# Kernel tuning notes

Hardware: AMD Instinct MI355X
Metric: run time of the kernel (lower is better)

## Reference

```python
import jax, jax.numpy as jnp
import numpy as np

HIDDEN = 4544
N_HEADS = 71
HEAD_DIM = 64
SEQ = 2048
ROPE_BASE = 10000.0


def _rope_cos_sin(seq_len, dim, base=ROPE_BASE):
    inv_freq = 1.0 / (base ** (jnp.arange(0, dim, 2, dtype=jnp.float32) / dim))
    t = jnp.arange(seq_len, dtype=jnp.float32)
    freqs = jnp.einsum('i,j->ij', t, inv_freq)          # [s, dim/2]
    emb = jnp.concatenate([freqs, freqs], axis=-1)      # [s, dim]
    return jnp.cos(emb), jnp.sin(emb)


def _rotate_half(x):
    x1, x2 = jnp.split(x, 2, axis=-1)
    return jnp.concatenate([-x2, x1], axis=-1)


def _apply_rope(x, cos, sin):
    # x: [..., s, d]; cos/sin: [s, d] broadcast over leading dims
    return x * cos + _rotate_half(x) * sin


def setup_inputs() -> dict:
    key = jax.random.key(0)
    k1, k2, k3 = jax.random.split(key, 3)
    hidden_states = jax.random.normal(k1, (1, 1, SEQ, HIDDEN), dtype=jnp.float32) * 0.02
    qkv_weight = jax.random.normal(k2, ((N_HEADS + 2) * HEAD_DIM, HIDDEN), dtype=jnp.float32) * 0.02
    dense_weight = jax.random.normal(k3, (HIDDEN, HIDDEN), dtype=jnp.float32) * 0.02
    # causal additive mask, same construction as the torch module (triu of -1e5)
    mask = jnp.triu(jnp.full((SEQ, SEQ), -100000.0, dtype=jnp.float32), k=1)[None, None]
    return {
        'hidden_states': hidden_states,
        'qkv_weight': qkv_weight,
        'dense_weight': dense_weight,
        'attention_mask': mask,
    }


def reference(hidden_states, qkv_weight, dense_weight, attention_mask):
    b = hidden_states.shape[0]
    s = hidden_states.shape[2]
    x = hidden_states[:, 0]                                   # [b, s, H]

    # fused QKV projection (no bias): [b, s, (nH+2)*d]
    fused = jnp.einsum('bsh,oh->bso', x, qkv_weight)

    q = fused[..., : N_HEADS * HEAD_DIM]
    q = q.reshape(b, s, N_HEADS, HEAD_DIM).transpose(0, 2, 1, 3)   # [b, nH, s, d]
    k = fused[..., N_HEADS * HEAD_DIM : (N_HEADS + 1) * HEAD_DIM]  # [b, s, d] (single KV head, MQA)
    v = fused[..., (N_HEADS + 1) * HEAD_DIM :]                     # [b, s, d]

    cos, sin = _rope_cos_sin(s, HEAD_DIM)
    q = _apply_rope(q, cos, sin)
    k = _apply_rope(k, cos, sin)

    scale = 1.0 / np.sqrt(HEAD_DIM).astype(np.float32)
    scores = jnp.einsum('bhqd,bkd->bhqk', q, k) * scale            # [b, nH, s, s]
    scores = scores + attention_mask
    attn = jax.nn.softmax(scores, axis=-1)
    out = jnp.einsum('bhqk,bkd->bhqd', attn, v)                    # [b, nH, s, d]

    out = out.transpose(0, 2, 1, 3).reshape(b, s, N_HEADS * HEAD_DIM)  # concat heads
    out = jnp.einsum('bsh,oh->bso', out, dense_weight)             # dense projection
    return out[:, None]                                            # [b, 1, s, H]
```

## Files before the change

kernel.cpp:

```cpp
#include <hip/hip_runtime.h>

#define SEQ     2048
#define HIDDEN  4544
#define NHEAD   71
#define HD      64
#define QKV_OUT 4672

typedef __bf16    bf16;
typedef _Float16  f16;
typedef __bf16    bf16x8 __attribute__((ext_vector_type(8)));
typedef __bf16    bf16x4 __attribute__((ext_vector_type(4)));
typedef _Float16  f16x4  __attribute__((ext_vector_type(4)));
typedef float     f32x4  __attribute__((ext_vector_type(4)));

__device__ inline void gl2lds16(const void* g, void* ldsbase) {
  __builtin_amdgcn_global_load_lds(
      (const __attribute__((address_space(1))) unsigned int*)g,
      (__attribute__((address_space(3))) unsigned int*)ldsbase,
      16, 0, 0);
}

__global__ void cvt_f32_bf16_k(const float* __restrict__ in, bf16* __restrict__ out, int n4) {
  int i = blockIdx.x * blockDim.x + threadIdx.x;
  if (i >= n4) return;
  float4 f = ((const float4*)in)[i];
  bf16x4 o;
  o[0] = (bf16)f.x; o[1] = (bf16)f.y; o[2] = (bf16)f.z; o[3] = (bf16)f.w;
  *(bf16x4*)(out + (size_t)i * 4) = o;
}

__global__ __launch_bounds__(256) void gemm_bt_k(const bf16* __restrict__ A,
                                                 const bf16* __restrict__ B,
                                                 float* __restrict__ C,
                                                 int K, int Nmat, int ldc) {
  __shared__ bf16 lA[2][128 * 32];
  __shared__ bf16 lB[2][128 * 32];
  const int t = threadIdx.x;
  const int lane = t & 63, w = t >> 6;
  const int m0 = blockIdx.x * 128, n0 = blockIdx.y * 128;
  const int wm = (w >> 1) * 64, wn = (w & 1) * 64;
  const int qi = lane & 15, grp = lane >> 4;

  const int r0 = t >> 2;
  const int c0 = (t & 3) * 8;
  const bf16* gA0 = A + (size_t)(m0 + r0) * K + c0;
  const bf16* gA1 = A + (size_t)(m0 + 64 + r0) * K + c0;
  int bR0 = n0 + r0;      if (bR0 >= Nmat) bR0 = Nmat - 1;
  int bR1 = n0 + 64 + r0; if (bR1 >= Nmat) bR1 = Nmat - 1;
  const bf16* gB0 = B + (size_t)bR0 * K + c0;
  const bf16* gB1 = B + (size_t)bR1 * K + c0;
  bf16* lA00 = &lA[0][0] + w * 512;
  bf16* lA01 = &lA[0][2048] + w * 512;
  bf16* lA10 = &lA[1][0] + w * 512;
  bf16* lA11 = &lA[1][2048] + w * 512;
  bf16* lB00 = &lB[0][0] + w * 512;
  bf16* lB01 = &lB[0][2048] + w * 512;
  bf16* lB10 = &lB[1][0] + w * 512;
  bf16* lB11 = &lB[1][2048] + w * 512;

  f32x4 acc[4][4] = {};
  for (int k0 = 0; k0 < K; k0 += 64) {
    __syncthreads();
    gl2lds16(gA0 + k0,      lA00);
    gl2lds16(gA1 + k0,      lA01);
    gl2lds16(gA0 + k0 + 32, lA10);
    gl2lds16(gA1 + k0 + 32, lA11);
    gl2lds16(gB0 + k0,      lB00);
    gl2lds16(gB1 + k0,      lB01);
    gl2lds16(gB0 + k0 + 32, lB10);
    gl2lds16(gB1 + k0 + 32, lB11);
    __syncthreads();
#pragma unroll
    for (int half = 0; half < 2; ++half) {
      bf16x8 af[4], bfv[4];
#pragma unroll
      for (int i = 0; i < 4; ++i)
        af[i] = *(const bf16x8*)&lA[half][(wm + i * 16 + qi) * 32 + grp * 8];
#pragma unroll
      for (int i = 0; i < 4; ++i)
        bfv[i] = *(const bf16x8*)&lB[half][(wn + i * 16 + qi) * 32 + grp * 8];
#pragma unroll
      for (int i = 0; i < 4; ++i)
#pragma unroll
        for (int j = 0; j < 4; ++j)
          acc[i][j] = __builtin_amdgcn_mfma_f32_16x16x32_bf16(af[i], bfv[j], acc[i][j], 0, 0, 0);
    }
  }

#pragma unroll
  for (int i = 0; i < 4; ++i) {
    const int row = m0 + wm + i * 16 + grp * 4;
#pragma unroll
    for (int j = 0; j < 4; ++j) {
      const int col = n0 + wn + j * 16 + qi;
      if (col < Nmat) {
#pragma unroll
        for (int r = 0; r < 4; ++r)
          C[(size_t)(row + r) * ldc + col] = acc[i][j][r];
      }
    }
  }
}

__global__ __launch_bounds__(256) void rope_q_k(const float* __restrict__ fused,
                                                bf16* __restrict__ Qb,
                                                float* __restrict__ cs_tab,
                                                float* __restrict__ sn_tab) {
  const int s = blockIdx.x, t = threadIdx.x;
  __shared__ float cs[64], sn[64];
  if (t < 64) {
    int i = t & 31;
    double invf = pow(10000.0, -(double)i / 32.0);
    double ang = (double)s * invf;
    float c = (float)cos(ang), n = (float)sin(ang);
    cs[t] = c; sn[t] = n;
    cs_tab[s * 64 + t] = c;
    sn_tab[s * 64 + t] = n;
  }
  __syncthreads();
  const float* row = fused + (size_t)s * QKV_OUT;
  for (int e = t; e < HIDDEN; e += 256) {
    int d = e & 63;
    float x = row[e], xp = row[e ^ 32];
    float rot = (d < 32) ? -xp : xp;
    Qb[(size_t)s * HIDDEN + e] = (bf16)((x * cs[d] + rot * sn[d]) * 0.125f);
  }
}

__global__ __launch_bounds__(64) void kvprep_k(const float* __restrict__ fused,
                                               const float* __restrict__ cs_tab,
                                               const float* __restrict__ sn_tab,
                                               bf16* __restrict__ Kf,
                                               f16* __restrict__ Vf) {
  const int t16 = blockIdx.x, lane = threadIdx.x;
  const int qi = lane & 15, grp = lane >> 4;
  const int s = t16 * 16 + qi;
  const float* krow = fused + (size_t)s * QKV_OUT + NHEAD * 64;
  const float* cs = cs_tab + s * 64;
  const float* sn = sn_tab + s * 64;
#pragma unroll
  for (int half = 0; half < 2; ++half) {
    bf16x8 o;
    const int d0 = half * 32 + grp * 8;
#pragma unroll
    for (int j = 0; j < 8; ++j) {
      int d = d0 + j;
      float x = krow[d], xp = krow[d ^ 32];
      float rot = (d < 32) ? -xp : xp;
      o[j] = (bf16)(x * cs[d] + rot * sn[d]);
    }
    *(bf16x8*)&Kf[(t16 * 2 + half) * 512 + lane * 8] = o;
  }
#pragma unroll
  for (int tt = 0; tt < 4; ++tt) {
    f16x4 o;
#pragma unroll
    for (int j = 0; j < 4; ++j)
      o[j] = (f16)fused[(size_t)(t16 * 16 + grp * 4 + j) * QKV_OUT + (NHEAD + 1) * 64 + tt * 16 + qi];
    *(f16x4*)&Vf[t16 * 1024 + tt * 256 + lane * 4] = o;
  }
}

__global__ __launch_bounds__(64) void attn_k(const bf16* __restrict__ Qb,
                                             const bf16* __restrict__ Kf,
                                             const f16*  __restrict__ Vf,
                                             bf16* __restrict__ Ao) {
  __shared__ float fl[2 * 16 * 68];
  const int h = blockIdx.y;
  const int b32 = gridDim.x - 1 - blockIdx.x;
  const int lane = threadIdx.x;
  const int qi = lane & 15, grp = lane >> 4;
  const int q0 = b32 * 32;
  const int lastT = b32 >> 1;

  bf16x8 qf[2][2];
#pragma unroll
  for (int qq = 0; qq < 2; ++qq) {
    const bf16* qb = Qb + (size_t)(q0 + qq * 16 + qi) * HIDDEN + h * 64 + grp * 8;
    qf[qq][0] = *(const bf16x8*)qb;
    qf[qq][1] = *(const bf16x8*)(qb + 32);
  }

  f32x4 o[2][4] = {};
  float l[2] = {0.f, 0.f};

  for (int kb = 0; kb <= lastT; ++kb) {
    const bf16* kfp = Kf + (size_t)kb * 4096 + lane * 8;
    bf16x8 kf[4][2];
#pragma unroll
    for (int kk = 0; kk < 4; ++kk) {
      kf[kk][0] = *(const bf16x8*)(kfp + kk * 1024);
      kf[kk][1] = *(const bf16x8*)(kfp + kk * 1024 + 512);
    }
    f32x4 s4[2][4];
#pragma unroll
    for (int qq = 0; qq < 2; ++qq)
#pragma unroll
      for (int kk = 0; kk < 4; ++kk) {
        f32x4 z = {};
        s4[qq][kk] = __builtin_amdgcn_mfma_f32_16x16x32_bf16(kf[kk][0], qf[qq][0], z, 0, 0, 0);
        s4[qq][kk] = __builtin_amdgcn_mfma_f32_16x16x32_bf16(kf[kk][1], qf[qq][1], s4[qq][kk], 0, 0, 0);
      }
    const f16* vfp = Vf + (size_t)kb * 4096 + lane * 4;
    f16x4 vf[4][4];
#pragma unroll
    for (int kk = 0; kk < 4; ++kk)
#pragma unroll
      for (int tt = 0; tt < 4; ++tt)
        vf[kk][tt] = *(const f16x4*)(vfp + kk * 1024 + tt * 256);

    if (kb == lastT) {
      const int dq = q0 - kb * 64 + qi;
#pragma unroll
      for (int qq = 0; qq < 2; ++qq)
#pragma unroll
        for (int kk = 0; kk < 4; ++kk)
#pragma unroll
          for (int r = 0; r < 4; ++r)
            if (kk * 16 + grp * 4 + r > dq + qq * 16) s4[qq][kk][r] = -1e30f;
    }
    f16x4 pf[2][4];
#pragma unroll
    for (int qq = 0; qq < 2; ++qq) {
      float ls = 0.f;
#pragma unroll
      for (int kk = 0; kk < 4; ++kk) {
        float p0 = __expf(s4[qq][kk][0]), p1 = __expf(s4[qq][kk][1]);
        float p2 = __expf(s4[qq][kk][2]), p3 = __expf(s4[qq][kk][3]);
        ls += (p0 + p1) + (p2 + p3);
        pf[qq][kk][0] = (f16)p0; pf[qq][kk][1] = (f16)p1;
        pf[qq][kk][2] = (f16)p2; pf[qq][kk][3] = (f16)p3;
      }
      l[qq] += ls;
    }
#pragma unroll
    for (int qq = 0; qq < 2; ++qq)
#pragma unroll
      for (int tt = 0; tt < 4; ++tt)
#pragma unroll
        for (int kk = 0; kk < 4; ++kk)
          o[qq][tt] = __builtin_amdgcn_mfma_f32_16x16x16f16(pf[qq][kk], vf[kk][tt], o[qq][tt], 0, 0, 0);
  }

#pragma unroll
  for (int qq = 0; qq < 2; ++qq) {
    float lq = l[qq];
    lq += __shfl_xor(lq, 16);
    lq += __shfl_xor(lq, 32);
    const float inv = 1.0f / lq;
    const float i0 = __shfl(inv, grp * 4 + 0);
    const float i1 = __shfl(inv, grp * 4 + 1);
    const float i2 = __shfl(inv, grp * 4 + 2);
    const float i3 = __shfl(inv, grp * 4 + 3);
    float* flq = fl + qq * 1088;
#pragma unroll
    for (int tt = 0; tt < 4; ++tt) {
      flq[(grp * 4 + 0) * 68 + tt * 16 + qi] = o[qq][tt][0] * i0;
      flq[(grp * 4 + 1) * 68 + tt * 16 + qi] = o[qq][tt][1] * i1;
      flq[(grp * 4 + 2) * 68 + tt * 16 + qi] = o[qq][tt][2] * i2;
      flq[(grp * 4 + 3) * 68 + tt * 16 + qi] = o[qq][tt][3] * i3;
    }
  }
  __syncthreads();
  const int row = lane >> 2, c0 = (lane & 3) * 16;
#pragma unroll
  for (int qq = 0; qq < 2; ++qq) {
    const float* flq = fl + qq * 1088;
    bf16x8 w0, w1;
#pragma unroll
    for (int j = 0; j < 8; ++j) {
      w0[j] = (bf16)flq[row * 68 + c0 + j];
      w1[j] = (bf16)flq[row * 68 + c0 + 8 + j];
    }
    bf16* ob = Ao + (size_t)(q0 + qq * 16 + row) * HIDDEN + h * 64 + c0;
    *(bf16x8*)ob = w0;
    *(bf16x8*)(ob + 8) = w1;
  }
}

extern "C" void kernel_launch(void* const* d_in, const int* in_sizes, int n_in,
                              void* d_out, int out_size, void* d_ws, size_t ws_size,
                              hipStream_t stream) {
  (void)in_sizes; (void)n_in; (void)out_size; (void)ws_size;
  const float* hs   = (const float*)d_in[0];
  const float* wqkv = (const float*)d_in[1];
  const float* wd   = (const float*)d_in[2];
  float* out = (float*)d_out;

  char* ws = (char*)d_ws;
  size_t off = 0;
  auto alloc = [&](size_t b) -> char* {
    char* p = ws + off;
    off += (b + 255) & ~(size_t)255;
    return p;
  };
  bf16* Xb     = (bf16*)alloc((size_t)SEQ * HIDDEN * 2);
  bf16* Wqb    = (bf16*)alloc((size_t)QKV_OUT * HIDDEN * 2);
  bf16* Wdb    = (bf16*)alloc((size_t)HIDDEN * HIDDEN * 2);
  float* fused = (float*)alloc((size_t)SEQ * QKV_OUT * 4);
  bf16* Qb     = (bf16*)alloc((size_t)SEQ * HIDDEN * 2);
  bf16* Kf     = (bf16*)alloc((size_t)(SEQ / 16) * 1024 * 2);
  f16*  Vf     = (f16*)alloc((size_t)(SEQ / 16) * 1024 * 2);
  float* cs_tab = (float*)alloc((size_t)SEQ * 64 * 4);
  float* sn_tab = (float*)alloc((size_t)SEQ * 64 * 4);
  bf16* Ao     = (bf16*)fused;

  {
    int n4 = SEQ * HIDDEN / 4;
    cvt_f32_bf16_k<<<(n4 + 255) / 256, 256, 0, stream>>>(hs, Xb, n4);
    n4 = QKV_OUT * HIDDEN / 4;
    cvt_f32_bf16_k<<<(n4 + 255) / 256, 256, 0, stream>>>(wqkv, Wqb, n4);
    n4 = HIDDEN * HIDDEN / 4;
    cvt_f32_bf16_k<<<(n4 + 255) / 256, 256, 0, stream>>>(wd, Wdb, n4);
  }
  gemm_bt_k<<<dim3(SEQ / 128, (QKV_OUT + 127) / 128), 256, 0, stream>>>(
      Xb, Wqb, fused, HIDDEN, QKV_OUT, QKV_OUT);
  rope_q_k<<<SEQ, 256, 0, stream>>>(fused, Qb, cs_tab, sn_tab);
  kvprep_k<<<SEQ / 16, 64, 0, stream>>>(fused, cs_tab, sn_tab, Kf, Vf);
  attn_k<<<dim3(SEQ / 32, NHEAD), 64, 0, stream>>>(Qb, Kf, Vf, Ao);
  gemm_bt_k<<<dim3(SEQ / 128, (HIDDEN + 127) / 128), 256, 0, stream>>>(
      Ao, Wdb, out, HIDDEN, HIDDEN, HIDDEN);
}
```

Baseline: 571.2 us.

## Split-K both GEMMs into two bf16 partials and reduce in finish kernels

Both projection GEMMs now run with a grid z-dimension of two, each half covering part of K (split at 2304), and write bf16 partial results to a workspace. A QKV finish kernel sums the partials, applies RoPE to Q and extracts raw K/V, and a dense finish kernel sums the partials into the fp32 output. The RoPE tables move into their own kernel. The aim is more blocks per GEMM to fill the CUs (16x37 and 16x36 tiles is fewer than two waves). In exchange it adds partial-buffer traffic, extra launches, and bf16 rounding of the partial sums.

Result: slower. 583.9 us (+2.2%).

```diff
diff --git a/kernel.cpp b/kernel.cpp
--- a/kernel.cpp
+++ b/kernel.cpp
@@ -5,6 +5,7 @@
 #define NHEAD   71
 #define HD      64
 #define QKV_OUT 4672
+#define KSPLIT  2304
 
 typedef __bf16    bf16;
 typedef _Float16  f16;
@@ -29,10 +30,21 @@
   *(bf16x4*)(out + (size_t)i * 4) = o;
 }
 
-__global__ __launch_bounds__(256) void gemm_bt_k(const bf16* __restrict__ A,
-                                                 const bf16* __restrict__ B,
-                                                 float* __restrict__ C,
-                                                 int K, int Nmat, int ldc) {
+__global__ __launch_bounds__(64) void tab_k(float* __restrict__ cs_tab,
+                                            float* __restrict__ sn_tab) {
+  const int s = blockIdx.x, t = threadIdx.x;
+  const int i = t & 31;
+  double invf = pow(10000.0, -(double)i / 32.0);
+  double ang = (double)s * invf;
+  cs_tab[s * 64 + t] = (float)cos(ang);
+  sn_tab[s * 64 + t] = (float)sin(ang);
+}
+
+__global__ __launch_bounds__(256) void gemm_bt_splitk(const bf16* __restrict__ A,
+                                                      const bf16* __restrict__ B,
+                                                      bf16* __restrict__ Cp,
+                                                      int K, int Nmat, int ldc,
+                                                      size_t partStride) {
   __shared__ bf16 lA[2][128 * 32];
   __shared__ bf16 lB[2][128 * 32];
   const int t = threadIdx.x;
@@ -40,6 +52,8 @@
   const int m0 = blockIdx.x * 128, n0 = blockIdx.y * 128;
   const int wm = (w >> 1) * 64, wn = (w & 1) * 64;
   const int qi = lane & 15, grp = lane >> 4;
+  const int kbeg = blockIdx.z ? KSPLIT : 0;
+  const int kend = blockIdx.z ? K : KSPLIT;
 
   const int r0 = t >> 2;
   const int c0 = (t & 3) * 8;
@@ -59,7 +73,7 @@
   bf16* lB11 = &lB[1][2048] + w * 512;
 
   f32x4 acc[4][4] = {};
-  for (int k0 = 0; k0 < K; k0 += 64) {
+  for (int k0 = kbeg; k0 < kend; k0 += 64) {
     __syncthreads();
     gl2lds16(gA0 + k0,      lA00);
     gl2lds16(gA1 + k0,      lA01);
@@ -87,6 +101,7 @@
     }
   }
 
+  bf16* Cz = Cp + blockIdx.z * partStride;
 #pragma unroll
   for (int i = 0; i < 4; ++i) {
     const int row = m0 + wm + i * 16 + grp * 4;
@@ -96,38 +111,36 @@
       if (col < Nmat) {
 #pragma unroll
         for (int r = 0; r < 4; ++r)
-          C[(size_t)(row + r) * ldc + col] = acc[i][j][r];
+          Cz[(size_t)(row + r) * ldc + col] = (bf16)acc[i][j][r];
       }
     }
   }
 }
 
-__global__ __launch_bounds__(256) void rope_q_k(const float* __restrict__ fused,
-                                                bf16* __restrict__ Qb,
-                                                float* __restrict__ cs_tab,
-                                                float* __restrict__ sn_tab) {
+__global__ __launch_bounds__(256) void qkv_finish_k(const bf16* __restrict__ P,
+                                                    size_t partStride,
+                                                    const float* __restrict__ cs_tab,
+                                                    const float* __restrict__ sn_tab,
+                                                    bf16* __restrict__ Qb,
+                                                    float* __restrict__ KVraw) {
   const int s = blockIdx.x, t = threadIdx.x;
   __shared__ float cs[64], sn[64];
-  if (t < 64) {
-    int i = t & 31;
-    double invf = pow(10000.0, -(double)i / 32.0);
-    double ang = (double)s * invf;
-    float c = (float)cos(ang), n = (float)sin(ang);
-    cs[t] = c; sn[t] = n;
-    cs_tab[s * 64 + t] = c;
-    sn_tab[s * 64 + t] = n;
-  }
+  if (t < 64) { cs[t] = cs_tab[s * 64 + t]; sn[t] = sn_tab[s * 64 + t]; }
   __syncthreads();
-  const float* row = fused + (size_t)s * QKV_OUT;
+  const bf16* r0 = P + (size_t)s * QKV_OUT;
+  const bf16* r1 = r0 + partStride;
   for (int e = t; e < HIDDEN; e += 256) {
-    int d = e & 63;
-    float x = row[e], xp = row[e ^ 32];
+    const int d = e & 63;
+    float x  = (float)r0[e] + (float)r1[e];
+    float xp = (float)r0[e ^ 32] + (float)r1[e ^ 32];
     float rot = (d < 32) ? -xp : xp;
     Qb[(size_t)s * HIDDEN + e] = (bf16)((x * cs[d] + rot * sn[d]) * 0.125f);
   }
-}
-
-__global__ __launch_bounds__(64) void kvprep_k(const float* __restrict__ fused,
+  if (t < 128)
+    KVraw[s * 128 + t] = (float)r0[HIDDEN + t] + (float)r1[HIDDEN + t];
+}
+
+__global__ __launch_bounds__(64) void kvprep_k(const float* __restrict__ KVraw,
                                                const float* __restrict__ cs_tab,
                                                const float* __restrict__ sn_tab,
                                                bf16* __restrict__ Kf,
@@ -135,7 +148,7 @@
   const int t16 = blockIdx.x, lane = threadIdx.x;
   const int qi = lane & 15, grp = lane >> 4;
   const int s = t16 * 16 + qi;
-  const float* krow = fused + (size_t)s * QKV_OUT + NHEAD * 64;
+  const float* krow = KVraw + (size_t)s * 128;
   const float* cs = cs_tab + s * 64;
   const float* sn = sn_tab + s * 64;
 #pragma unroll
@@ -156,7 +169,7 @@
     f16x4 o;
 #pragma unroll
     for (int j = 0; j < 4; ++j)
-      o[j] = (f16)fused[(size_t)(t16 * 16 + grp * 4 + j) * QKV_OUT + (NHEAD + 1) * 64 + tt * 16 + qi];
+      o[j] = (f16)KVraw[(size_t)(t16 * 16 + grp * 4 + j) * 128 + 64 + tt * 16 + qi];
     *(f16x4*)&Vf[t16 * 1024 + tt * 256 + lane * 4] = o;
   }
 }
@@ -278,6 +291,21 @@
   }
 }
 
+__global__ void dense_finish_k(const bf16* __restrict__ P, size_t partStride,
+                               float* __restrict__ out, int n8) {
+  int i = blockIdx.x * blockDim.x + threadIdx.x;
+  if (i >= n8) return;
+  bf16x8 a = *(const bf16x8*)(P + (size_t)i * 8);
+  bf16x8 b = *(const bf16x8*)(P + partStride + (size_t)i * 8);
+  float4 o0, o1;
+  o0.x = (float)a[0] + (float)b[0]; o0.y = (float)a[1] + (float)b[1];
+  o0.z = (float)a[2] + (float)b[2]; o0.w = (float)a[3] + (float)b[3];
+  o1.x = (float)a[4] + (float)b[4]; o1.y = (float)a[5] + (float)b[5];
+  o1.z = (float)a[6] + (float)b[6]; o1.w = (float)a[7] + (float)b[7];
+  ((float4*)out)[i * 2]     = o0;
+  ((float4*)out)[i * 2 + 1] = o1;
+}
+
 extern "C" void kernel_launch(void* const* d_in, const int* in_sizes, int n_in,
                               void* d_out, int out_size, void* d_ws, size_t ws_size,
                               hipStream_t stream) {
@@ -297,13 +325,14 @@
   bf16* Xb     = (bf16*)alloc((size_t)SEQ * HIDDEN * 2);
   bf16* Wqb    = (bf16*)alloc((size_t)QKV_OUT * HIDDEN * 2);
   bf16* Wdb    = (bf16*)alloc((size_t)HIDDEN * HIDDEN * 2);
-  float* fused = (float*)alloc((size_t)SEQ * QKV_OUT * 4);
+  bf16* Part   = (bf16*)alloc((size_t)2 * SEQ * QKV_OUT * 2);
   bf16* Qb     = (bf16*)alloc((size_t)SEQ * HIDDEN * 2);
   bf16* Kf     = (bf16*)alloc((size_t)(SEQ / 16) * 1024 * 2);
   f16*  Vf     = (f16*)alloc((size_t)(SEQ / 16) * 1024 * 2);
+  float* KVraw  = (float*)alloc((size_t)SEQ * 128 * 4);
   float* cs_tab = (float*)alloc((size_t)SEQ * 64 * 4);
   float* sn_tab = (float*)alloc((size_t)SEQ * 64 * 4);
-  bf16* Ao     = (bf16*)fused;
+  bf16* Ao     = Wqb;
 
   {
     int n4 = SEQ * HIDDEN / 4;
@@ -313,11 +342,18 @@
     n4 = HIDDEN * HIDDEN / 4;
     cvt_f32_bf16_k<<<(n4 + 255) / 256, 256, 0, stream>>>(wd, Wdb, n4);
   }
-  gemm_bt_k<<<dim3(SEQ / 128, (QKV_OUT + 127) / 128), 256, 0, stream>>>(
-      Xb, Wqb, fused, HIDDEN, QKV_OUT, QKV_OUT);
-  rope_q_k<<<SEQ, 256, 0, stream>>>(fused, Qb, cs_tab, sn_tab);
-  kvprep_k<<<SEQ / 16, 64, 0, stream>>>(fused, cs_tab, sn_tab, Kf, Vf);
+  tab_k<<<SEQ, 64, 0, stream>>>(cs_tab, sn_tab);
+
+  const size_t strideQ = (size_t)SEQ * QKV_OUT;
+  gemm_bt_splitk<<<dim3(SEQ / 128, (QKV_OUT + 127) / 128, 2), 256, 0, stream>>>(
+      Xb, Wqb, Part, HIDDEN, QKV_OUT, QKV_OUT, strideQ);
+  qkv_finish_k<<<SEQ, 256, 0, stream>>>(Part, strideQ, cs_tab, sn_tab, Qb, KVraw);
+  kvprep_k<<<SEQ / 16, 64, 0, stream>>>(KVraw, cs_tab, sn_tab, Kf, Vf);
   attn_k<<<dim3(SEQ / 32, NHEAD), 64, 0, stream>>>(Qb, Kf, Vf, Ao);
-  gemm_bt_k<<<dim3(SEQ / 128, (HIDDEN + 127) / 128), 256, 0, stream>>>(
-      Ao, Wdb, out, HIDDEN, HIDDEN, HIDDEN);
-}
+
+  const size_t strideD = (size_t)SEQ * HIDDEN;
+  gemm_bt_splitk<<<dim3(SEQ / 128, (HIDDEN + 127) / 128, 2), 256, 0, stream>>>(
+      Ao, Wdb, Part, HIDDEN, HIDDEN, HIDDEN, strideD);
+  dense_finish_k<<<(SEQ * HIDDEN / 8 + 255) / 256, 256, 0, stream>>>(
+      Part, strideD, out, SEQ * HIDDEN / 8);
+}
```
